# Kernel optimization log

Measured on AMD Instinct MI355X. Metric: run time of the kernel, lower is better.

## Reference

```python
import jax, jax.numpy as jnp
import numpy as np


def setup_inputs() -> dict:
    key = jax.random.key(0)
    k1, k2 = jax.random.split(key)
    query = jax.random.normal(k1, (16, 256, 32, 32), dtype=jnp.float32)
    search_map = jax.random.normal(k2, (16, 256, 64, 64), dtype=jnp.float32)
    return {"query": query, "search_map": search_map}


def reference(query, search_map):
    # query: [bs, c, h, w]; search_map: [bs, c, H, W]
    bs, c, h, w = query.shape
    # pad H and W by h//2, w//2 on each side (matches F.pad(left,right,top,bottom))
    padded = jnp.pad(search_map, ((0, 0), (0, 0), (h // 2, h // 2), (w // 2, w // 2)))

    def corr_one(map_, q_):
        # map_: [c, Hp, Wp], q_: [c, h, w]
        # per-sample cross-correlation: the query acts as a single-output conv kernel
        out = jax.lax.conv_general_dilated(
            map_[None],            # [1, c, Hp, Wp]
            q_[None],              # [1, c, h, w] -> OIHW
            window_strides=(1, 1),
            padding="VALID",
            dimension_numbers=("NCHW", "OIHW", "NCHW"),
        )
        return out[0]              # [1, Hout, Wout]

    # vmap over the batch: each sample uses its own query as the kernel
    return jax.vmap(corr_one)(padded, query)  # [bs, 1, Hout, Wout]
```

## Files before the change

### kernel.cpp

```cpp
#include <hip/hip_runtime.h>
#include <stdint.h>

typedef __bf16 bf16x8 __attribute__((ext_vector_type(8)));
typedef float  f32x4  __attribute__((ext_vector_type(4)));
typedef uint32_t u32x4 __attribute__((ext_vector_type(4)));

__device__ __forceinline__ uint16_t f2bf(float f) {
    uint32_t u = __builtin_bit_cast(uint32_t, f);
    u += 0x7FFFu + ((u >> 16) & 1u);
    return (uint16_t)(u >> 16);
}

__global__ __launch_bounds__(256) void qtrans_kernel(const float* __restrict__ Q,
                                                     uint16_t* __restrict__ Qt,
                                                     float* __restrict__ P) {
    __shared__ float T[8 * 1064];
    const int ch = blockIdx.x, b = blockIdx.y;
    const int tid = threadIdx.x;

    {
        const f32x4 z = {};
        f32x4* P4 = (f32x4*)P;
        size_t base = (size_t)(b * 32 + ch) * 1280 + tid;
        #pragma unroll
        for (int k = 0; k < 5; ++k) P4[base + k * 256] = z;
    }

    const float* src = Q + ((size_t)(b * 256 + ch * 8)) * 1024;
    #pragma unroll
    for (int it = 0; it < 8; ++it) {
        int idx4 = tid + it * 256;
        int c8 = idx4 >> 8, rem4 = idx4 & 255;
        f32x4 v = *(const f32x4*)(src + (size_t)c8 * 1024 + rem4 * 4);
        int i = (rem4 * 4) >> 5, j = (rem4 * 4) & 31;
        float* tr = &T[c8 * 1064 + i * 33 + j];
        tr[0] = v[0]; tr[1] = v[1]; tr[2] = v[2]; tr[3] = v[3];
    }
    __syncthreads();

    uint32_t* dst = (uint32_t*)Qt;
    #pragma unroll
    for (int it = 0; it < 16; ++it) {
        int o2 = tid + it * 256;
        int t  = (o2 & 3) * 2;
        int il = (o2 >> 2) & 15;
        int j  = (o2 >> 6) & 31;
        int ih = (o2 >> 11) & 1;
        float v0 = T[t * 1064 + (ih * 16 + il) * 33 + j];
        float v1 = T[(t + 1) * 1064 + (ih * 16 + il) * 33 + j];
        uint32_t pk = (uint32_t)f2bf(v0) | ((uint32_t)f2bf(v1) << 16);
        size_t oi = ((((size_t)(b * 2 + ih) * 32 + j) * 32 + ch) * 16 + il) * 4 + (t >> 1);
        dst[oi] = pk;
    }
}

__global__ __launch_bounds__(256, 3) void corr_kernel(const float* __restrict__ S,
                                                      const uint16_t* __restrict__ Qt,
                                                      float* __restrict__ P) {
    __shared__ __align__(16) char smem[40960];
    uint16_t* S_l = (uint16_t*)smem;
    float*    Pw  = (float*)smem;

    const int dp   = blockIdx.x;
    const int half = blockIdx.y;
    const int b    = blockIdx.z;
    const int tid = threadIdx.x, wave = tid >> 6, lane = tid & 63;
    const int l15 = lane & 15, l4 = lane >> 4;

    {
        const u32x4 z = {};
        for (int zi = tid; zi < 512; zi += 256) {
            int t = zi >> 8, ch = (zi >> 4) & 15, r = zi & 15;
            *(u32x4*)&S_l[t * 10240 + ch * 640 + r * 8] = z;
        }
    }
    {
        const int sx = tid & 63, w = tid >> 6;
        const int tile = w >> 1;
        const int chw  = (w & 1) * 8;
        const int d    = dp * 2 + tile;
        const float* sp = S + ((size_t)(b * 256 + half * 128)) * 4096 + (size_t)d * 64;
        #pragma unroll
        for (int k = 0; k < 8; ++k) {
            int chl = chw + k;
            float v[8];
            #pragma unroll
            for (int cc = 0; cc < 8; ++cc)
                v[cc] = sp[(size_t)(chl * 8 + cc) * 4096 + sx];
            u32x4 pk;
            #pragma unroll
            for (int q = 0; q < 4; ++q)
                pk[q] = (uint32_t)f2bf(v[2 * q]) | ((uint32_t)f2bf(v[2 * q + 1]) << 16);
            *(u32x4*)&S_l[tile * 10240 + chl * 640 + (sx + 16) * 8] = pk;
        }
    }
    __syncthreads();

    f32x4 acc[2][5][2] = {};

    const uint16_t* qb0 = Qt + (((size_t)b * 2 + 0) * 32) * 4096 + (half * 16 + l4) * 128 + l15 * 8;
    const uint16_t* qb1 = qb0 + 32 * 4096;

    bf16x8 Bc[4], Bn[4];
    {
        const size_t oa = (size_t)wave * 4096;
        Bc[0] = *(const bf16x8*)(qb0 + oa);
        Bc[1] = *(const bf16x8*)(qb1 + oa);
        Bc[2] = *(const bf16x8*)(qb0 + oa + 16 * 4096);
        Bc[3] = *(const bf16x8*)(qb1 + oa + 16 * 4096);
    }

    #pragma unroll
    for (int jj = 0; jj < 4; ++jj) {
        const int j0a = wave + jj * 4;
        int rowt[5];
        #pragma unroll
        for (int t = 0; t < 5; ++t) {
            int rr = j0a + t * 16 + l15;
            rowt[t] = (rr < 80) ? rr : 0;
        }

        #pragma unroll
        for (int s = 0; s < 4; ++s) {
            int njj = jj, ns = s + 1;
            if (ns == 4) { njj = jj + 1; ns = 0; }
            if (njj < 4) {
                const size_t o = (size_t)(wave + njj * 4) * 4096 + ns * 512;
                Bn[0] = *(const bf16x8*)(qb0 + o);
                Bn[1] = *(const bf16x8*)(qb1 + o);
                Bn[2] = *(const bf16x8*)(qb0 + o + 16 * 4096);
                Bn[3] = *(const bf16x8*)(qb1 + o + 16 * 4096);
            }

            const int chb = (s * 4 + l4) * 640;
            bf16x8 A[2][5];
            #pragma unroll
            for (int tile = 0; tile < 2; ++tile)
                #pragma unroll
                for (int t = 0; t < 5; ++t)
                    A[tile][t] = *(const bf16x8*)&S_l[tile * 10240 + chb + rowt[t] * 8];

            #pragma unroll
            for (int tile = 0; tile < 2; ++tile) {
                #pragma unroll
                for (int t = 0; t < 5; ++t) {
                    acc[tile][t][0] = __builtin_amdgcn_mfma_f32_16x16x32_bf16(A[tile][t], Bc[0], acc[tile][t][0], 0, 0, 0);
                    acc[tile][t][1] = __builtin_amdgcn_mfma_f32_16x16x32_bf16(A[tile][t], Bc[1], acc[tile][t][1], 0, 0, 0);
                }
                #pragma unroll
                for (int t = 1; t < 5; ++t) {
                    acc[tile][t - 1][0] = __builtin_amdgcn_mfma_f32_16x16x32_bf16(A[tile][t], Bc[2], acc[tile][t - 1][0], 0, 0, 0);
                    acc[tile][t - 1][1] = __builtin_amdgcn_mfma_f32_16x16x32_bf16(A[tile][t], Bc[3], acc[tile][t - 1][1], 0, 0, 0);
                }
            }
            Bc[0] = Bn[0]; Bc[1] = Bn[1]; Bc[2] = Bn[2]; Bc[3] = Bn[3];
        }
    }

    #pragma unroll
    for (int tile = 0; tile < 2; ++tile) {
        const int d = dp * 2 + tile;
        __syncthreads();
        {
            float* pw = Pw + wave * 2560;
            #pragma unroll
            for (int m = 0; m < 5; ++m)
                #pragma unroll
                for (int n = 0; n < 2; ++n)
                    *(f32x4*)&pw[(n * 16 + l15) * 80 + m * 16 + l4 * 4] = acc[tile][m][n];
        }
        __syncthreads();
        float* Pd = P + (size_t)(b * 64 + d) * 2560;
        for (int e = tid; e < 2560; e += 256) {
            float v = Pw[e] + Pw[2560 + e] + Pw[5120 + e] + Pw[7680 + e];
            atomicAdd(Pd + e, v);
        }
    }
}

__global__ __launch_bounds__(128) void reduce_kernel(const float* __restrict__ P,
                                                     float* __restrict__ out) {
    const int y = blockIdx.x, b = blockIdx.y;
    const int x = threadIdx.x;
    if (x >= 65) return;
    int ilo = 16 - y; if (ilo < 0) ilo = 0;
    int ihi = 80 - y; if (ihi > 32) ihi = 32;
    float s = 0.f;
    const float* Pb = P + (size_t)b * (64 * 2560) + x;
    for (int i = ilo; i < ihi; ++i)
        s += Pb[(size_t)(y + i - 16) * 2560 + i * 80];
    out[(size_t)b * 4225 + (size_t)y * 65 + x] = s;
}

__global__ __launch_bounds__(256) void naive_kernel(const float* __restrict__ Q,
                                                    const float* __restrict__ S,
                                                    float* __restrict__ out) {
    int gid = blockIdx.x * 256 + threadIdx.x;
    if (gid >= 67600) return;
    int b = gid / 4225, r = gid % 4225, y = r / 65, x = r % 65;
    int jlo = 16 - x; if (jlo < 0) jlo = 0;
    int jhi = 80 - x; if (jhi > 32) jhi = 32;
    float acc = 0.f;
    for (int c = 0; c < 256; ++c) {
        const float* Sb = S + ((size_t)(b * 256 + c)) * 4096;
        const float* Qb = Q + ((size_t)(b * 256 + c)) * 1024;
        for (int i = 0; i < 32; ++i) {
            int dd = y + i - 16;
            if ((unsigned)dd >= 64u) continue;
            const float* Sr = Sb + dd * 64 + (x - 16);
            const float* Qr = Qb + i * 32;
            for (int j = jlo; j < jhi; ++j) acc += Sr[j] * Qr[j];
        }
    }
    out[gid] = acc;
}

extern "C" void kernel_launch(void* const* d_in, const int* in_sizes, int n_in,
                              void* d_out, int out_size, void* d_ws, size_t ws_size,
                              hipStream_t stream) {
    (void)in_sizes; (void)n_in; (void)out_size;
    const float* Q = (const float*)d_in[0];
    const float* S = (const float*)d_in[1];
    float* out = (float*)d_out;

    const size_t QT_BYTES = (size_t)16 * 2 * 32 * 32 * 16 * 8 * 2;
    const size_t P_BYTES  = (size_t)16 * 64 * 32 * 80 * 4;

    if (ws_size < QT_BYTES + P_BYTES) {
        naive_kernel<<<(67600 + 255) / 256, 256, 0, stream>>>(Q, S, out);
        return;
    }
    uint16_t* Qt = (uint16_t*)d_ws;
    float*    P  = (float*)((char*)d_ws + QT_BYTES);

    qtrans_kernel<<<dim3(32, 16), 256, 0, stream>>>(Q, Qt, P);
    corr_kernel<<<dim3(32, 2, 16), 256, 0, stream>>>(S, Qt, P);
    reduce_kernel<<<dim3(65, 16), 128, 0, stream>>>(P, out);
}
```

Baseline: 147.0 us.

## Process one search row per block to shrink LDS and raise occupancy

Each corr_kernel block now handles a single search-map row instead of two, halving LDS to 20KB and the accumulator array, and the grid doubles to 64 blocks in x. Launch bounds go from 3 to 8 blocks per CU. The register double-buffer prefetch of query fragments is removed in favour of direct loads each step. The cross-wave reduction now folds waves 2-3 into waves 1-2 in shared memory before the atomics. The trade-off is twice as many blocks each re-reading the query data, and exposed global-load latency that now relies on occupancy to hide.

Measured after the change: 366.5 us. +149.4%, slower.

```diff
diff --git a/kernel.cpp b/kernel.cpp
--- a/kernel.cpp
+++ b/kernel.cpp
@@ -54,14 +54,14 @@
     }
 }
 
-__global__ __launch_bounds__(256, 3) void corr_kernel(const float* __restrict__ S,
+__global__ __launch_bounds__(256, 8) void corr_kernel(const float* __restrict__ S,
                                                       const uint16_t* __restrict__ Qt,
                                                       float* __restrict__ P) {
-    __shared__ __align__(16) char smem[40960];
+    __shared__ __align__(16) char smem[20480];
     uint16_t* S_l = (uint16_t*)smem;
     float*    Pw  = (float*)smem;
 
-    const int dp   = blockIdx.x;
+    const int d    = blockIdx.x;
     const int half = blockIdx.y;
     const int b    = blockIdx.z;
     const int tid = threadIdx.x, wave = tid >> 6, lane = tid & 63;
@@ -69,20 +69,18 @@
 
     {
         const u32x4 z = {};
-        for (int zi = tid; zi < 512; zi += 256) {
-            int t = zi >> 8, ch = (zi >> 4) & 15, r = zi & 15;
-            *(u32x4*)&S_l[t * 10240 + ch * 640 + r * 8] = z;
+        if (tid < 256) {
+            int zi = tid;
+            int ch = zi >> 4, r = zi & 15;
+            *(u32x4*)&S_l[ch * 640 + r * 8] = z;
         }
     }
     {
         const int sx = tid & 63, w = tid >> 6;
-        const int tile = w >> 1;
-        const int chw  = (w & 1) * 8;
-        const int d    = dp * 2 + tile;
         const float* sp = S + ((size_t)(b * 256 + half * 128)) * 4096 + (size_t)d * 64;
         #pragma unroll
-        for (int k = 0; k < 8; ++k) {
-            int chl = chw + k;
+        for (int k = 0; k < 4; ++k) {
+            int chl = w * 4 + k;
             float v[8];
             #pragma unroll
             for (int cc = 0; cc < 8; ++cc)
@@ -91,28 +89,23 @@
             #pragma unroll
             for (int q = 0; q < 4; ++q)
                 pk[q] = (uint32_t)f2bf(v[2 * q]) | ((uint32_t)f2bf(v[2 * q + 1]) << 16);
-            *(u32x4*)&S_l[tile * 10240 + chl * 640 + (sx + 16) * 8] = pk;
-        }
-    }
-    __syncthreads();
-
-    f32x4 acc[2][5][2] = {};
-
-    const uint16_t* qb0 = Qt + (((size_t)b * 2 + 0) * 32) * 4096 + (half * 16 + l4) * 128 + l15 * 8;
-    const uint16_t* qb1 = qb0 + 32 * 4096;
-
-    bf16x8 Bc[4], Bn[4];
-    {
-        const size_t oa = (size_t)wave * 4096;
-        Bc[0] = *(const bf16x8*)(qb0 + oa);
-        Bc[1] = *(const bf16x8*)(qb1 + oa);
-        Bc[2] = *(const bf16x8*)(qb0 + oa + 16 * 4096);
-        Bc[3] = *(const bf16x8*)(qb1 + oa + 16 * 4096);
-    }
+            *(u32x4*)&S_l[chl * 640 + (sx + 16) * 8] = pk;
+        }
+    }
+    __syncthreads();
+
+    f32x4 acc[5][2] = {};
 
     #pragma unroll
     for (int jj = 0; jj < 4; ++jj) {
         const int j0a = wave + jj * 4;
+        const uint16_t* qa0 = Qt + (((size_t)b * 2 + 0) * 32 + j0a) * 4096
+                                 + (half * 16 + l4) * 128 + l15 * 8;
+        const uint16_t* qa1 = Qt + (((size_t)b * 2 + 1) * 32 + j0a) * 4096
+                                 + (half * 16 + l4) * 128 + l15 * 8;
+        const uint16_t* qb0 = qa0 + 16 * 4096;
+        const uint16_t* qb1 = qa1 + 16 * 4096;
+
         int rowt[5];
         #pragma unroll
         for (int t = 0; t < 5; ++t) {
@@ -122,59 +115,55 @@
 
         #pragma unroll
         for (int s = 0; s < 4; ++s) {
-            int njj = jj, ns = s + 1;
-            if (ns == 4) { njj = jj + 1; ns = 0; }
-            if (njj < 4) {
-                const size_t o = (size_t)(wave + njj * 4) * 4096 + ns * 512;
-                Bn[0] = *(const bf16x8*)(qb0 + o);
-                Bn[1] = *(const bf16x8*)(qb1 + o);
-                Bn[2] = *(const bf16x8*)(qb0 + o + 16 * 4096);
-                Bn[3] = *(const bf16x8*)(qb1 + o + 16 * 4096);
+            bf16x8 Ba0 = *(const bf16x8*)(qa0 + s * 512);
+            bf16x8 Ba1 = *(const bf16x8*)(qa1 + s * 512);
+            bf16x8 Bb0 = *(const bf16x8*)(qb0 + s * 512);
+            bf16x8 Bb1 = *(const bf16x8*)(qb1 + s * 512);
+            const int chb = (s * 4 + l4) * 640;
+            bf16x8 A[5];
+            #pragma unroll
+            for (int t = 0; t < 5; ++t)
+                A[t] = *(const bf16x8*)&S_l[chb + rowt[t] * 8];
+            #pragma unroll
+            for (int t = 0; t < 5; ++t) {
+                acc[t][0] = __builtin_amdgcn_mfma_f32_16x16x32_bf16(A[t], Ba0, acc[t][0], 0, 0, 0);
+                acc[t][1] = __builtin_amdgcn_mfma_f32_16x16x32_bf16(A[t], Ba1, acc[t][1], 0, 0, 0);
             }
-
-            const int chb = (s * 4 + l4) * 640;
-            bf16x8 A[2][5];
-            #pragma unroll
-            for (int tile = 0; tile < 2; ++tile)
-                #pragma unroll
-                for (int t = 0; t < 5; ++t)
-                    A[tile][t] = *(const bf16x8*)&S_l[tile * 10240 + chb + rowt[t] * 8];
-
-            #pragma unroll
-            for (int tile = 0; tile < 2; ++tile) {
-                #pragma unroll
-                for (int t = 0; t < 5; ++t) {
-                    acc[tile][t][0] = __builtin_amdgcn_mfma_f32_16x16x32_bf16(A[tile][t], Bc[0], acc[tile][t][0], 0, 0, 0);
-                    acc[tile][t][1] = __builtin_amdgcn_mfma_f32_16x16x32_bf16(A[tile][t], Bc[1], acc[tile][t][1], 0, 0, 0);
-                }
-                #pragma unroll
-                for (int t = 1; t < 5; ++t) {
-                    acc[tile][t - 1][0] = __builtin_amdgcn_mfma_f32_16x16x32_bf16(A[tile][t], Bc[2], acc[tile][t - 1][0], 0, 0, 0);
-                    acc[tile][t - 1][1] = __builtin_amdgcn_mfma_f32_16x16x32_bf16(A[tile][t], Bc[3], acc[tile][t - 1][1], 0, 0, 0);
-                }
+            #pragma unroll
+            for (int t = 1; t < 5; ++t) {
+                acc[t - 1][0] = __builtin_amdgcn_mfma_f32_16x16x32_bf16(A[t], Bb0, acc[t - 1][0], 0, 0, 0);
+                acc[t - 1][1] = __builtin_amdgcn_mfma_f32_16x16x32_bf16(A[t], Bb1, acc[t - 1][1], 0, 0, 0);
             }
-            Bc[0] = Bn[0]; Bc[1] = Bn[1]; Bc[2] = Bn[2]; Bc[3] = Bn[3];
-        }
-    }
-
-    #pragma unroll
-    for (int tile = 0; tile < 2; ++tile) {
-        const int d = dp * 2 + tile;
-        __syncthreads();
-        {
-            float* pw = Pw + wave * 2560;
-            #pragma unroll
-            for (int m = 0; m < 5; ++m)
-                #pragma unroll
-                for (int n = 0; n < 2; ++n)
-                    *(f32x4*)&pw[(n * 16 + l15) * 80 + m * 16 + l4 * 4] = acc[tile][m][n];
-        }
-        __syncthreads();
-        float* Pd = P + (size_t)(b * 64 + d) * 2560;
-        for (int e = tid; e < 2560; e += 256) {
-            float v = Pw[e] + Pw[2560 + e] + Pw[5120 + e] + Pw[7680 + e];
-            atomicAdd(Pd + e, v);
-        }
+        }
+    }
+
+    __syncthreads();
+    if (wave < 2) {
+        float* pw = Pw + wave * 2560;
+        #pragma unroll
+        for (int m = 0; m < 5; ++m)
+            #pragma unroll
+            for (int n = 0; n < 2; ++n)
+                *(f32x4*)&pw[(n * 16 + l15) * 80 + m * 16 + l4 * 4] = acc[m][n];
+    }
+    __syncthreads();
+    if (wave >= 2) {
+        float* pw = Pw + (wave - 2) * 2560;
+        #pragma unroll
+        for (int m = 0; m < 5; ++m)
+            #pragma unroll
+            for (int n = 0; n < 2; ++n) {
+                float* p = &pw[(n * 16 + l15) * 80 + m * 16 + l4 * 4];
+                f32x4 t = *(f32x4*)p;
+                t += acc[m][n];
+                *(f32x4*)p = t;
+            }
+    }
+    __syncthreads();
+    float* Pd = P + (size_t)(b * 64 + d) * 2560;
+    for (int e = tid; e < 2560; e += 256) {
+        float v = Pw[e] + Pw[2560 + e];
+        atomicAdd(Pd + e, v);
     }
 }
 
@@ -234,6 +223,6 @@
     float*    P  = (float*)((char*)d_ws + QT_BYTES);
 
     qtrans_kernel<<<dim3(32, 16), 256, 0, stream>>>(Q, Qt, P);
-    corr_kernel<<<dim3(32, 2, 16), 256, 0, stream>>>(S, Qt, P);
+    corr_kernel<<<dim3(64, 2, 16), 256, 0, stream>>>(S, Qt, P);
     reduce_kernel<<<dim3(65, 16), 128, 0, stream>>>(P, out);
 }
```
